# Kernel tuning notes

Measured on AMD Instinct MI355X. Metric: run time of the kernel, lower is better.

The kernel has to match this reference:

```python
import jax, jax.numpy as jnp
import numpy as np

B, S, D = 8, 2048, 512

def setup_inputs() -> dict:
    key = jax.random.key(0)
    ks = jax.random.split(key, 9)
    scale = 1.0 / np.sqrt(D)
    q = jax.random.normal(ks[0], (B, S, D), dtype=jnp.float32)
    k = jax.random.normal(ks[1], (B, S, D), dtype=jnp.float32)
    v = jax.random.normal(ks[2], (B, S, D), dtype=jnp.float32)
    # causal mask, broadcast over batch: True = attend
    mask = jnp.tril(jnp.ones((S, S), dtype=bool))[None, :, :]
    Wq = jax.random.normal(ks[3], (D, D), dtype=jnp.float32) * scale
    bq = jax.random.normal(ks[4], (D,), dtype=jnp.float32) * scale
    Wk = jax.random.normal(ks[5], (D, D), dtype=jnp.float32) * scale
    bk = jax.random.normal(ks[6], (D,), dtype=jnp.float32) * scale
    Wv = jax.random.normal(ks[7], (D, D), dtype=jnp.float32) * scale
    bv = jax.random.normal(ks[8], (D,), dtype=jnp.float32) * scale
    return {"q": q, "k": k, "v": v, "mask": mask,
            "Wq": Wq, "bq": bq, "Wk": Wk, "bk": bk, "Wv": Wv, "bv": bv}

def reference(q, k, v, mask, Wq, bq, Wk, bk, Wv, bv):
    # torch nn.Linear: x @ W^T + b
    Q = jnp.einsum('bsd,ed->bse', q, Wq) + bq
    K = jnp.einsum('bsd,ed->bse', k, Wk) + bk
    V = jnp.einsum('bsd,ed->bse', v, Wv) + bv
    scores = jnp.einsum('bqd,bkd->bqk', Q, K) / jnp.sqrt(jnp.float32(D))
    scores = jnp.where(mask, scores, jnp.float32(-1e9))
    prob = jax.nn.softmax(scores, axis=-1)
    out = jnp.einsum('bqk,bkd->bqd', prob, V)
    return out
```

## Files before the change

kernel.cpp:

```cpp
#include <hip/hip_runtime.h>
#include <stdint.h>
#include <stddef.h>

typedef _Float16 half8 __attribute__((ext_vector_type(8)));
typedef float f32x4 __attribute__((ext_vector_type(4)));

#define SCALE_QK 0.04419417382415922f

__device__ __forceinline__ void gload16(const void* g, void* lds) {
  __builtin_amdgcn_global_load_lds(
      (const __attribute__((address_space(1))) void*)g,
      (__attribute__((address_space(3))) void*)lds,
      16, 0, 0);
}

template<bool A_F32>
__device__ __forceinline__ void run_kloop(const void* Arow0, const _Float16* Brow0,
                                          int lda, int ldb, int kIters,
                                          _Float16 (*As)[128*64], _Float16 (*Bs)[128*64],
                                          f32x4 (&acc)[4][4])
{
  const int tid  = threadIdx.x;
  const int lane = tid & 63;
  const int w    = tid >> 6;
  const int wm   = w >> 1, wn = w & 1;
  const int srow = tid >> 3;
  const int sg   = tid & 7;
  const int swz  = sg ^ (srow & 7);
  const int fr   = lane & 15;
  const int fq   = lane >> 4;
  const int fx   = lane & 7;

  f32x4 pre0[8], pre1[8];

  auto issueA32 = [&](int it, f32x4 (&dst)[8]) {
    const float* A = (const float*)Arow0;
    const int k0 = it * 64;
    #pragma unroll
    for (int i = 0; i < 4; ++i) {
      const float* src = A + (size_t)(i*32 + srow) * lda + (k0 + sg*8);
      dst[2*i]   = *(const f32x4*)src;
      dst[2*i+1] = *(const f32x4*)(src + 4);
    }
  };
  auto writeA32 = [&](const f32x4 (&src)[8], _Float16* dstAs) {
    #pragma unroll
    for (int i = 0; i < 4; ++i) {
      f32x4 x = src[2*i], y = src[2*i+1];
      half8 h;
      h[0]=(_Float16)x[0]; h[1]=(_Float16)x[1]; h[2]=(_Float16)x[2]; h[3]=(_Float16)x[3];
      h[4]=(_Float16)y[0]; h[5]=(_Float16)y[1]; h[6]=(_Float16)y[2]; h[7]=(_Float16)y[3];
      *(half8*)(dstAs + (i*32 + srow)*64 + swz*8) = h;
    }
  };
  auto gloadA16 = [&](int it, _Float16* dstAs) {
    const _Float16* A = (const _Float16*)Arow0;
    const int k0 = it * 64;
    #pragma unroll
    for (int i = 0; i < 4; ++i)
      gload16(A + (size_t)(i*32 + srow) * lda + (k0 + swz*8), dstAs + i*2048 + w*512);
  };
  auto gloadB = [&](int it, _Float16* dstBs) {
    const int k0 = it * 64;
    #pragma unroll
    for (int i = 0; i < 4; ++i)
      gload16(Brow0 + (size_t)(i*32 + srow) * ldb + (k0 + swz*8), dstBs + i*2048 + w*512);
  };
  auto compute = [&](const _Float16* cAs, const _Float16* cBs) {
    #pragma unroll
    for (int ks = 0; ks < 2; ++ks) {
      half8 av[4], bv[4];
      const int slot = (ks*4 + fq) ^ fx;
      #pragma unroll
      for (int i = 0; i < 4; ++i) {
        av[i] = *(const half8*)(cAs + (wm*64 + i*16 + fr)*64 + slot*8);
        bv[i] = *(const half8*)(cBs + (wn*64 + i*16 + fr)*64 + slot*8);
      }
      #pragma unroll
      for (int i = 0; i < 4; ++i) {
        #pragma unroll
        for (int j = 0; j < 4; ++j)
          acc[i][j] = __builtin_amdgcn_mfma_f32_16x16x32_f16(av[i], bv[j], acc[i][j], 0, 0, 0);
      }
    }
  };
  auto kstep = [&](int it, _Float16* curAs, _Float16* curBs,
                   _Float16* nxtAs, _Float16* nxtBs,
                   f32x4 (&pCons)[8], f32x4 (&pIss)[8]) {
    const bool more = (it + 1) < kIters;
    if (more) {
      gloadB(it + 1, nxtBs);
      if constexpr (!A_F32) gloadA16(it + 1, nxtAs);
      else if (it + 2 < kIters) issueA32(it + 2, pIss);
    }
    compute(curAs, curBs);
    if (more) { if constexpr (A_F32) writeA32(pCons, nxtAs); }
    __syncthreads();
  };

  if constexpr (A_F32) {
    issueA32(0, pre0);
    gloadB(0, Bs[0]);
    writeA32(pre0, As[0]);
    if (kIters > 1) issueA32(1, pre1);
  } else {
    gloadA16(0, As[0]);
    gloadB(0, Bs[0]);
  }
  __syncthreads();

  for (int it = 0; it < kIters; it += 2) {
    kstep(it,     As[0], Bs[0], As[1], Bs[1], pre1, pre0);
    kstep(it + 1, As[1], Bs[1], As[0], Bs[0], pre0, pre1);
  }
}

__global__ __launch_bounds__(256) void k_cvtw(const float* __restrict__ Wq,
                                              const float* __restrict__ Wk,
                                              const float* __restrict__ Wv,
                                              _Float16* __restrict__ Wb)
{
  const int t = blockIdx.x * 256 + threadIdx.x;
  const int base = t * 8;
  const int z = base >> 18;
  const int off = base & 262143;
  const float* src = (z == 0) ? Wq : ((z == 1) ? Wk : Wv);
  f32x4 a = *(const f32x4*)(src + off);
  f32x4 b = *(const f32x4*)(src + off + 4);
  half8 h;
  h[0]=(_Float16)a[0]; h[1]=(_Float16)a[1]; h[2]=(_Float16)a[2]; h[3]=(_Float16)a[3];
  h[4]=(_Float16)b[0]; h[5]=(_Float16)b[1]; h[6]=(_Float16)b[2]; h[7]=(_Float16)b[3];
  *(half8*)(Wb + base) = h;
}

__global__ __launch_bounds__(256) void k_proj(const float* __restrict__ q,
                                              const float* __restrict__ k,
                                              const float* __restrict__ v,
                                              const _Float16* __restrict__ Wb,
                                              const float* __restrict__ bq,
                                              const float* __restrict__ bk,
                                              const float* __restrict__ bv,
                                              _Float16* __restrict__ Qb,
                                              _Float16* __restrict__ Kb,
                                              _Float16* __restrict__ Vb)
{
  __shared__ __align__(16) _Float16 As[2][128*64];
  __shared__ __align__(16) _Float16 Bs[2][128*64];
  const int z = blockIdx.z;
  const float* A     = (z == 0) ? q  : (z == 1) ? k  : v;
  const float* bia   = (z == 0) ? bq : (z == 1) ? bk : bv;
  const _Float16* B  = Wb + (size_t)z * 512 * 512;
  _Float16* C        = (z == 0) ? Qb : (z == 1) ? Kb : Vb;
  const int mt = blockIdx.y, nt = blockIdx.x;

  f32x4 acc[4][4] = {};
  run_kloop<true>(A + (size_t)mt*128*512, B + (size_t)nt*128*512, 512, 512, 8, As, Bs, acc);

  const int lane = threadIdx.x & 63, w = threadIdx.x >> 6;
  const int wm = w >> 1, wn = w & 1;
  const int fr = lane & 15, fq = lane >> 4;
  #pragma unroll
  for (int j = 0; j < 4; ++j) {
    const int col = nt*128 + wn*64 + j*16 + fr;
    const float bval = bia[col];
    #pragma unroll
    for (int i = 0; i < 4; ++i) {
      const int row = mt*128 + wm*64 + i*16 + fq*4;
      #pragma unroll
      for (int r = 0; r < 4; ++r)
        C[(size_t)(row + r) * 512 + col] = (_Float16)(acc[i][j][r] + bval);
    }
  }
}

__global__ __launch_bounds__(256) void k_trans(const _Float16* __restrict__ Vb,
                                               _Float16* __restrict__ Vt)
{
  __shared__ __align__(16) _Float16 t[64][72];
  const int st = blockIdx.x, dt = blockIdx.y, b = blockIdx.z;
  const int r = threadIdx.x >> 2, g = threadIdx.x & 3;
  const _Float16* src = Vb + ((size_t)b*2048 + st*64 + r)*512 + dt*64 + g*16;
  half8 v0 = *(const half8*)src;
  half8 v1 = *(const half8*)(src + 8);
  *(half8*)&t[r][g*16]     = v0;
  *(half8*)&t[r][g*16 + 8] = v1;
  __syncthreads();
  half8 o0, o1;
  #pragma unroll
  for (int i2 = 0; i2 < 8; ++i2) o0[i2] = t[g*16 + i2][r];
  #pragma unroll
  for (int i2 = 0; i2 < 8; ++i2) o1[i2] = t[g*16 + 8 + i2][r];
  _Float16* dst = Vt + ((size_t)b*512 + dt*64 + r)*2048 + st*64 + g*16;
  *(half8*)dst       = o0;
  *(half8*)(dst + 8) = o1;
}

__global__ __launch_bounds__(256) void k_scores(const _Float16* __restrict__ Qb,
                                                const _Float16* __restrict__ Kb,
                                                _Float16* __restrict__ P)
{
  const int kt = blockIdx.x, qt = blockIdx.y, b = blockIdx.z;
  if (kt > qt) return;
  __shared__ __align__(16) _Float16 As[2][128*64];
  __shared__ __align__(16) _Float16 Bs[2][128*64];
  f32x4 acc[4][4] = {};
  run_kloop<false>(Qb + ((size_t)b*2048 + qt*128)*512,
                   Kb + ((size_t)b*2048 + kt*128)*512,
                   512, 512, 8, As, Bs, acc);
  const int lane = threadIdx.x & 63, w = threadIdx.x >> 6;
  const int wm = w >> 1, wn = w & 1;
  const int fr = lane & 15, fq = lane >> 4;
  #pragma unroll
  for (int i = 0; i < 4; ++i) {
    const int row = qt*128 + wm*64 + i*16 + fq*4;
    #pragma unroll
    for (int j = 0; j < 4; ++j) {
      const int col = kt*128 + wn*64 + j*16 + fr;
      #pragma unroll
      for (int r = 0; r < 4; ++r)
        P[((size_t)b*2048 + row + r) * 2048 + col] = (_Float16)(acc[i][j][r] * SCALE_QK);
    }
  }
}

__global__ __launch_bounds__(256) void k_softmax(_Float16* __restrict__ P)
{
  const int lane = threadIdx.x & 63;
  const int row  = blockIdx.x * 4 + (threadIdx.x >> 6);
  const int qIdx = row & 2047;
  _Float16* p = P + (size_t)row * 2048;
  const int L    = qIdx + 1;
  const int Lpad = ((qIdx >> 7) + 1) * 128;

  float m = -1e30f, s = 0.f;
  for (int i0 = lane * 8; i0 < L; i0 += 512) {
    float xv[8];
    if (i0 + 8 <= L) {
      half8 x = *(const half8*)(p + i0);
      #pragma unroll
      for (int j = 0; j < 8; ++j) xv[j] = (float)x[j];
    } else {
      #pragma unroll
      for (int j = 0; j < 8; ++j) xv[j] = (i0 + j < L) ? (float)p[i0 + j] : -1e30f;
    }
    float cm = xv[0];
    #pragma unroll
    for (int j = 1; j < 8; ++j) cm = fmaxf(cm, xv[j]);
    const float mn = fmaxf(m, cm);
    float cs = 0.f;
    #pragma unroll
    for (int j = 0; j < 8; ++j) cs += __expf(xv[j] - mn);
    s = s * __expf(m - mn) + cs;
    m = mn;
  }
  #pragma unroll
  for (int d = 1; d < 64; d <<= 1) {
    const float mo = __shfl_xor(m, d, 64);
    const float so = __shfl_xor(s, d, 64);
    const float mn = fmaxf(m, mo);
    s = s * __expf(m - mn) + so * __expf(mo - mn);
    m = mn;
  }
  const float inv = 1.0f / s;

  for (int i0 = lane * 8; i0 < Lpad; i0 += 512) {
    half8 o;
    if (i0 + 8 <= L) {
      half8 x = *(const half8*)(p + i0);
      #pragma unroll
      for (int j = 0; j < 8; ++j) o[j] = (_Float16)(__expf((float)x[j] - m) * inv);
    } else {
      #pragma unroll
      for (int j = 0; j < 8; ++j) {
        const int idx = i0 + j;
        o[j] = (idx < L) ? (_Float16)(__expf((float)p[idx] - m) * inv) : (_Float16)0.f;
      }
    }
    *(half8*)(p + i0) = o;
  }
}

__global__ __launch_bounds__(256) void k_pv(const _Float16* __restrict__ P,
                                            const _Float16* __restrict__ Vt,
                                            float* __restrict__ Out)
{
  const int dt = blockIdx.x, b = blockIdx.z;
  const int yr = blockIdx.y;
  const int qt = (yr & 1) ? (15 - (yr >> 1)) : (yr >> 1);
  __shared__ __align__(16) _Float16 As[2][128*64];
  __shared__ __align__(16) _Float16 Bs[2][128*64];
  f32x4 acc[4][4] = {};
  run_kloop<false>(P  + ((size_t)b*2048 + qt*128)*2048,
                   Vt + ((size_t)b*512  + dt*128)*2048,
                   2048, 2048, (qt + 1) * 2, As, Bs, acc);
  const int lane = threadIdx.x & 63, w = threadIdx.x >> 6;
  const int wm = w >> 1, wn = w & 1;
  const int fr = lane & 15, fq = lane >> 4;
  #pragma unroll
  for (int i = 0; i < 4; ++i) {
    const int row = qt*128 + wm*64 + i*16 + fq*4;
    #pragma unroll
    for (int j = 0; j < 4; ++j) {
      const int col = dt*128 + wn*64 + j*16 + fr;
      #pragma unroll
      for (int r = 0; r < 4; ++r)
        Out[((size_t)b*2048 + row + r) * 512 + col] = acc[i][j][r];
    }
  }
}

extern "C" void kernel_launch(void* const* d_in, const int* in_sizes, int n_in,
                              void* d_out, int out_size, void* d_ws, size_t ws_size,
                              hipStream_t stream) {
  (void)in_sizes; (void)n_in; (void)out_size;
  const float* q  = (const float*)d_in[0];
  const float* k  = (const float*)d_in[1];
  const float* v  = (const float*)d_in[2];
  const float* Wq = (const float*)d_in[4];
  const float* bq = (const float*)d_in[5];
  const float* Wk = (const float*)d_in[6];
  const float* bk = (const float*)d_in[7];
  const float* Wv = (const float*)d_in[8];
  const float* bv = (const float*)d_in[9];

  const size_t OFF_P  = 0;
  const size_t OFF_Q  = (size_t)64 << 20;
  const size_t OFF_K  = (size_t)80 << 20;
  const size_t OFF_V  = (size_t)96 << 20;
  const size_t OFF_VT = (size_t)112 << 20;
  const size_t OFF_W  = (size_t)128 << 20;
  const size_t NEEDED = OFF_W + (size_t)3 * 512 * 512 * sizeof(_Float16);
  if (ws_size < NEEDED) return;

  char* ws = (char*)d_ws;
  _Float16* P  = (_Float16*)(ws + OFF_P);
  _Float16* Qb = (_Float16*)(ws + OFF_Q);
  _Float16* Kb = (_Float16*)(ws + OFF_K);
  _Float16* Vb = (_Float16*)(ws + OFF_V);
  _Float16* Vt = (_Float16*)(ws + OFF_VT);
  _Float16* Wb = (_Float16*)(ws + OFF_W);
  float* Out = (float*)d_out;

  k_cvtw   <<<dim3(384),       dim3(256), 0, stream>>>(Wq, Wk, Wv, Wb);
  k_proj   <<<dim3(4, 128, 3), dim3(256), 0, stream>>>(q, k, v, Wb, bq, bk, bv, Qb, Kb, Vb);
  k_trans  <<<dim3(32, 8, 8),  dim3(256), 0, stream>>>(Vb, Vt);
  k_scores <<<dim3(16, 16, 8), dim3(256), 0, stream>>>(Qb, Kb, P);
  k_softmax<<<dim3(4096),      dim3(256), 0, stream>>>(P);
  k_pv     <<<dim3(4, 16, 8),  dim3(256), 0, stream>>>(P, Vt, Out);
}
```

Baseline: 326.4 us.

## Single-buffer A tile, remap grids for XCD locality and compact causal scores launch

Measured after the change: 282.8 us. 13.4% less time.

```diff
diff --git a/kernel.cpp b/kernel.cpp
--- a/kernel.cpp
+++ b/kernel.cpp
@@ -1,6 +1,7 @@
 #include <hip/hip_runtime.h>
 #include <stdint.h>
 #include <stddef.h>
+#include <math.h>
 
 typedef _Float16 half8 __attribute__((ext_vector_type(8)));
 typedef float f32x4 __attribute__((ext_vector_type(4)));
@@ -17,7 +18,7 @@
 template<bool A_F32>
 __device__ __forceinline__ void run_kloop(const void* Arow0, const _Float16* Brow0,
                                           int lda, int ldb, int kIters,
-                                          _Float16 (*As)[128*64], _Float16 (*Bs)[128*64],
+                                          _Float16* As, _Float16 (*Bs)[128*64],
                                           f32x4 (&acc)[4][4])
 {
   const int tid  = threadIdx.x;
@@ -31,34 +32,39 @@
   const int fq   = lane >> 4;
   const int fx   = lane & 7;
 
-  f32x4 pre0[8], pre1[8];
-
-  auto issueA32 = [&](int it, f32x4 (&dst)[8]) {
-    const float* A = (const float*)Arow0;
+  f32x4 preF[8];
+  half8 preH[4];
+
+  auto loadA = [&](int it) {
     const int k0 = it * 64;
+    if constexpr (A_F32) {
+      const float* A = (const float*)Arow0;
+      #pragma unroll
+      for (int i = 0; i < 4; ++i) {
+        const float* src = A + (size_t)(i*32 + srow) * lda + (k0 + sg*8);
+        preF[2*i]   = *(const f32x4*)src;
+        preF[2*i+1] = *(const f32x4*)(src + 4);
+      }
+    } else {
+      const _Float16* A = (const _Float16*)Arow0;
+      #pragma unroll
+      for (int i = 0; i < 4; ++i)
+        preH[i] = *(const half8*)(A + (size_t)(i*32 + srow) * lda + (k0 + sg*8));
+    }
+  };
+  auto writeA = [&]() {
     #pragma unroll
     for (int i = 0; i < 4; ++i) {
-      const float* src = A + (size_t)(i*32 + srow) * lda + (k0 + sg*8);
-      dst[2*i]   = *(const f32x4*)src;
-      dst[2*i+1] = *(const f32x4*)(src + 4);
-    }
-  };
-  auto writeA32 = [&](const f32x4 (&src)[8], _Float16* dstAs) {
-    #pragma unroll
-    for (int i = 0; i < 4; ++i) {
-      f32x4 x = src[2*i], y = src[2*i+1];
       half8 h;
-      h[0]=(_Float16)x[0]; h[1]=(_Float16)x[1]; h[2]=(_Float16)x[2]; h[3]=(_Float16)x[3];
-      h[4]=(_Float16)y[0]; h[5]=(_Float16)y[1]; h[6]=(_Float16)y[2]; h[7]=(_Float16)y[3];
-      *(half8*)(dstAs + (i*32 + srow)*64 + swz*8) = h;
-    }
-  };
-  auto gloadA16 = [&](int it, _Float16* dstAs) {
-    const _Float16* A = (const _Float16*)Arow0;
-    const int k0 = it * 64;
-    #pragma unroll
-    for (int i = 0; i < 4; ++i)
-      gload16(A + (size_t)(i*32 + srow) * lda + (k0 + swz*8), dstAs + i*2048 + w*512);
+      if constexpr (A_F32) {
+        f32x4 x = preF[2*i], y = preF[2*i+1];
+        h[0]=(_Float16)x[0]; h[1]=(_Float16)x[1]; h[2]=(_Float16)x[2]; h[3]=(_Float16)x[3];
+        h[4]=(_Float16)y[0]; h[5]=(_Float16)y[1]; h[6]=(_Float16)y[2]; h[7]=(_Float16)y[3];
+      } else {
+        h = preH[i];
+      }
+      *(half8*)(As + (i*32 + srow)*64 + swz*8) = h;
+    }
   };
   auto gloadB = [&](int it, _Float16* dstBs) {
     const int k0 = it * 64;
@@ -66,14 +72,14 @@
     for (int i = 0; i < 4; ++i)
       gload16(Brow0 + (size_t)(i*32 + srow) * ldb + (k0 + swz*8), dstBs + i*2048 + w*512);
   };
-  auto compute = [&](const _Float16* cAs, const _Float16* cBs) {
+  auto compute = [&](const _Float16* cBs) {
     #pragma unroll
     for (int ks = 0; ks < 2; ++ks) {
       half8 av[4], bv[4];
       const int slot = (ks*4 + fq) ^ fx;
       #pragma unroll
       for (int i = 0; i < 4; ++i) {
-        av[i] = *(const half8*)(cAs + (wm*64 + i*16 + fr)*64 + slot*8);
+        av[i] = *(const half8*)(As + (wm*64 + i*16 + fr)*64 + slot*8);
         bv[i] = *(const half8*)(cBs + (wn*64 + i*16 + fr)*64 + slot*8);
       }
       #pragma unroll
@@ -84,34 +90,23 @@
       }
     }
   };
-  auto kstep = [&](int it, _Float16* curAs, _Float16* curBs,
-                   _Float16* nxtAs, _Float16* nxtBs,
-                   f32x4 (&pCons)[8], f32x4 (&pIss)[8]) {
+
+  loadA(0);
+  gloadB(0, Bs[0]);
+  writeA();
+  __syncthreads();
+
+  for (int it = 0; it < kIters; ++it) {
+    const int cur = it & 1;
     const bool more = (it + 1) < kIters;
     if (more) {
-      gloadB(it + 1, nxtBs);
-      if constexpr (!A_F32) gloadA16(it + 1, nxtAs);
-      else if (it + 2 < kIters) issueA32(it + 2, pIss);
-    }
-    compute(curAs, curBs);
-    if (more) { if constexpr (A_F32) writeA32(pCons, nxtAs); }
+      gloadB(it + 1, Bs[cur ^ 1]);
+      loadA(it + 1);
+    }
+    compute(Bs[cur]);
     __syncthreads();
-  };
-
-  if constexpr (A_F32) {
-    issueA32(0, pre0);
-    gloadB(0, Bs[0]);
-    writeA32(pre0, As[0]);
-    if (kIters > 1) issueA32(1, pre1);
-  } else {
-    gloadA16(0, As[0]);
-    gloadB(0, Bs[0]);
-  }
-  __syncthreads();
-
-  for (int it = 0; it < kIters; it += 2) {
-    kstep(it,     As[0], Bs[0], As[1], Bs[1], pre1, pre0);
-    kstep(it + 1, As[1], Bs[1], As[0], Bs[0], pre0, pre1);
+    if (more) writeA();
+    __syncthreads();
   }
 }
 
@@ -144,14 +139,18 @@
                                               _Float16* __restrict__ Kb,
                                               _Float16* __restrict__ Vb)
 {
-  __shared__ __align__(16) _Float16 As[2][128*64];
+  __shared__ __align__(16) _Float16 As[128*64];
   __shared__ __align__(16) _Float16 Bs[2][128*64];
-  const int z = blockIdx.z;
+  const int bid = blockIdx.x;
+  const int xcd = bid & 7, i = bid >> 3;
+  const int p = xcd * 48 + (i >> 2);
+  const int nt = i & 3;
+  const int z = p >> 7, mt = p & 127;
+
   const float* A     = (z == 0) ? q  : (z == 1) ? k  : v;
   const float* bia   = (z == 0) ? bq : (z == 1) ? bk : bv;
   const _Float16* B  = Wb + (size_t)z * 512 * 512;
   _Float16* C        = (z == 0) ? Qb : (z == 1) ? Kb : Vb;
-  const int mt = blockIdx.y, nt = blockIdx.x;
 
   f32x4 acc[4][4] = {};
   run_kloop<true>(A + (size_t)mt*128*512, B + (size_t)nt*128*512, 512, 512, 8, As, Bs, acc);
@@ -164,11 +163,11 @@
     const int col = nt*128 + wn*64 + j*16 + fr;
     const float bval = bia[col];
     #pragma unroll
-    for (int i = 0; i < 4; ++i) {
-      const int row = mt*128 + wm*64 + i*16 + fq*4;
+    for (int i2 = 0; i2 < 4; ++i2) {
+      const int row = mt*128 + wm*64 + i2*16 + fq*4;
       #pragma unroll
       for (int r = 0; r < 4; ++r)
-        C[(size_t)(row + r) * 512 + col] = (_Float16)(acc[i][j][r] + bval);
+        C[(size_t)(row + r) * 512 + col] = (_Float16)(acc[i2][j][r] + bval);
     }
   }
 }
@@ -199,9 +198,16 @@
                                                 const _Float16* __restrict__ Kb,
                                                 _Float16* __restrict__ P)
 {
-  const int kt = blockIdx.x, qt = blockIdx.y, b = blockIdx.z;
-  if (kt > qt) return;
-  __shared__ __align__(16) _Float16 As[2][128*64];
+  const int bid = blockIdx.x;
+  const int b = bid & 7;
+  const int t = bid >> 3;
+  int qt = (int)((sqrtf(8.0f * (float)t + 1.0f) - 1.0f) * 0.5f);
+  int base = (qt * (qt + 1)) >> 1;
+  if (t < base)                { --qt; base = (qt * (qt + 1)) >> 1; }
+  else if (t >= base + qt + 1) { ++qt; base = (qt * (qt + 1)) >> 1; }
+  const int kt = t - base;
+
+  __shared__ __align__(16) _Float16 As[128*64];
   __shared__ __align__(16) _Float16 Bs[2][128*64];
   f32x4 acc[4][4] = {};
   run_kloop<false>(Qb + ((size_t)b*2048 + qt*128)*512,
@@ -284,10 +290,13 @@
                                             const _Float16* __restrict__ Vt,
                                             float* __restrict__ Out)
 {
-  const int dt = blockIdx.x, b = blockIdx.z;
-  const int yr = blockIdx.y;
-  const int qt = (yr & 1) ? (15 - (yr >> 1)) : (yr >> 1);
-  __shared__ __align__(16) _Float16 As[2][128*64];
+  const int bid = blockIdx.x;
+  const int b = bid & 7;
+  const int r0 = bid >> 3;
+  const int qi = r0 >> 2, dt = r0 & 3;
+  const int qt = (qi & 1) ? (15 - (qi >> 1)) : (qi >> 1);
+
+  __shared__ __align__(16) _Float16 As[128*64];
   __shared__ __align__(16) _Float16 Bs[2][128*64];
   f32x4 acc[4][4] = {};
   run_kloop<false>(P  + ((size_t)b*2048 + qt*128)*2048,
@@ -341,10 +350,10 @@
   _Float16* Wb = (_Float16*)(ws + OFF_W);
   float* Out = (float*)d_out;
 
-  k_cvtw   <<<dim3(384),       dim3(256), 0, stream>>>(Wq, Wk, Wv, Wb);
-  k_proj   <<<dim3(4, 128, 3), dim3(256), 0, stream>>>(q, k, v, Wb, bq, bk, bv, Qb, Kb, Vb);
-  k_trans  <<<dim3(32, 8, 8),  dim3(256), 0, stream>>>(Vb, Vt);
-  k_scores <<<dim3(16, 16, 8), dim3(256), 0, stream>>>(Qb, Kb, P);
-  k_softmax<<<dim3(4096),      dim3(256), 0, stream>>>(P);
-  k_pv     <<<dim3(4, 16, 8),  dim3(256), 0, stream>>>(P, Vt, Out);
-}
+  k_cvtw   <<<dim3(384),      dim3(256), 0, stream>>>(Wq, Wk, Wv, Wb);
+  k_proj   <<<dim3(1536),     dim3(256), 0, stream>>>(q, k, v, Wb, bq, bk, bv, Qb, Kb, Vb);
+  k_trans  <<<dim3(32, 8, 8), dim3(256), 0, stream>>>(Vb, Vt);
+  k_scores <<<dim3(1088),     dim3(256), 0, stream>>>(Qb, Kb, P);
+  k_softmax<<<dim3(4096),     dim3(256), 0, stream>>>(P);
+  k_pv     <<<dim3(512),      dim3(256), 0, stream>>>(P, Vt, Out);
+}
```
